# Kernel tuning notes

Hardware: AMD Instinct MI355X
Metric: run time of the kernel (lower is better)

The kernel has to match this reference:

```python
import jax, jax.numpy as jnp
import numpy as np
import math

D = 768
H = 8
DK = D // H
FF = 1024
EPS = 1e-5


def _layer_norm(x, g, b):
    m = jnp.mean(x, axis=-1, keepdims=True)
    v = jnp.mean((x - m) ** 2, axis=-1, keepdims=True)
    return (x - m) * jax.lax.rsqrt(v + EPS) * g + b


def _mha(x, attention_mask, Wq, bq, Wv, bv, g, b):
    # x: (B,S,D); attention_mask: (B,S,1) bool (True = masked/padding query row)
    B, S, _ = x.shape
    q = (x @ Wq + bq).reshape(B, S, H, DK).transpose(0, 2, 1, 3)  # (B,H,S,dk)
    # NOTE: original code uses the V projection for BOTH k and v (k = self.V(x))
    kv = (x @ Wv + bv).reshape(B, S, H, DK).transpose(0, 2, 1, 3)
    k = kv
    v = kv
    w = jnp.einsum('bhqd,bhkd->bhqk', q, k) / math.sqrt(DK)  # (B,H,S,S)
    pad = attention_mask[:, None, :, :]                      # (B,1,S,1) -> bcast (B,1,S,S)
    causal = jnp.triu(jnp.ones((S, S), dtype=bool), k=1)     # look-ahead mask
    mask = pad | causal
    w = jnp.where(mask, jnp.float32(-1e9), w)
    # NOTE: original uses nn.Softmax(dim=2) -> softmax over the QUERY axis
    score = jax.nn.softmax(w, axis=2)
    o = jnp.einsum('bhqk,bhkd->bhqd', score, v)              # (B,H,S,dk)
    o = o.transpose(0, 2, 1, 3).reshape(B, S, D)
    return _layer_norm(o + x, g, b)


def _ffn(x, W1, b1, W2, b2, g, b):
    h = jax.nn.relu(x @ W1 + b1)
    return _layer_norm(h @ W2 + b2 + x, g, b)


def setup_inputs() -> dict:
    key = jax.random.key(0)
    ks = jax.random.split(key, 16)
    B, S = 8, 1024
    sc = 0.02
    inp = {
        'x': jax.random.normal(ks[0], (B, S, D), dtype=jnp.float32),
        'attention_mask': jax.random.randint(ks[1], (B, S, 1), 0, 2).astype(bool),
    }
    for i, pre in enumerate(['a1', 'a2']):
        inp[pre + '_Wq'] = jax.random.normal(ks[2 + 4 * i], (D, D), dtype=jnp.float32) * sc
        inp[pre + '_bq'] = jnp.zeros((D,), dtype=jnp.float32)
        inp[pre + '_Wv'] = jax.random.normal(ks[3 + 4 * i], (D, D), dtype=jnp.float32) * sc
        inp[pre + '_bv'] = jnp.zeros((D,), dtype=jnp.float32)
        inp[pre + '_g'] = jnp.ones((D,), dtype=jnp.float32)
        inp[pre + '_b'] = jnp.zeros((D,), dtype=jnp.float32)
    inp['f_W1'] = jax.random.normal(ks[10], (D, FF), dtype=jnp.float32) * sc
    inp['f_b1'] = jnp.zeros((FF,), dtype=jnp.float32)
    inp['f_W2'] = jax.random.normal(ks[11], (FF, D), dtype=jnp.float32) * sc
    inp['f_b2'] = jnp.zeros((D,), dtype=jnp.float32)
    inp['f_g'] = jnp.ones((D,), dtype=jnp.float32)
    inp['f_b'] = jnp.zeros((D,), dtype=jnp.float32)
    return inp


def reference(x, attention_mask,
              a1_Wq, a1_bq, a1_Wv, a1_bv, a1_g, a1_b,
              a2_Wq, a2_bq, a2_Wv, a2_bv, a2_g, a2_b,
              f_W1, f_b1, f_W2, f_b2, f_g, f_b):
    x = _mha(x, attention_mask, a1_Wq, a1_bq, a1_Wv, a1_bv, a1_g, a1_b)
    x = _mha(x, attention_mask, a2_Wq, a2_bq, a2_Wv, a2_bv, a2_g, a2_b)
    x = _ffn(x, f_W1, f_b1, f_W2, f_b2, f_g, f_b)
    return x
```

## Files before the change

kernel.cpp:

```cpp
#include <hip/hip_runtime.h>
#include <cstddef>

#define BB 8
#define SS 1024
#define DD 768
#define HH 8
#define DKK 96
#define FFF 1024
#define MM (BB*SS)
#define QVW 1536
#define SM_SCALE 0.10206207261596577f
#define NT2 8

typedef unsigned short ushort_t;
typedef short short8 __attribute__((ext_vector_type(8)));
typedef float f32x4 __attribute__((ext_vector_type(4)));
typedef float f32x16 __attribute__((ext_vector_type(16)));
typedef ushort_t us4 __attribute__((ext_vector_type(4)));
typedef unsigned uint2v __attribute__((ext_vector_type(2)));

__device__ __forceinline__ ushort_t f2b(float f) {
    union { float f; unsigned u; } x; x.f = f;
    unsigned r = x.u + 0x7fffu + ((x.u >> 16) & 1u);
    return (ushort_t)(r >> 16);
}
__device__ __forceinline__ float b2f(ushort_t u) {
    union { unsigned u; float f; } x; x.u = ((unsigned)u) << 16;
    return x.f;
}
__device__ __forceinline__ void gload16(const ushort_t* g, void* lds_base) {
    __builtin_amdgcn_global_load_lds(
        (const __attribute__((address_space(1))) unsigned int*)g,
        (__attribute__((address_space(3))) unsigned int*)lds_base, 16, 0, 0);
}
__device__ __forceinline__ void plswap(unsigned& a, unsigned& b) {
#if __has_builtin(__builtin_amdgcn_permlane32_swap)
    uint2v r = __builtin_amdgcn_permlane32_swap(a, b, false, false);
    a = r[0]; b = r[1];
#else
    asm("v_permlane32_swap_b32 %0, %1" : "+v"(a), "+v"(b));
#endif
}

__device__ __forceinline__ void castWT_body(
    const float* __restrict__ W, ushort_t* __restrict__ Wt,
    int K, int N, int bx, int by)
{
    __shared__ float T[32][33];
    const int tx = threadIdx.x & 31, ty = threadIdx.x >> 5;
    const int n0 = bx * 32, k0 = by * 32;
    #pragma unroll
    for (int r = 0; r < 4; ++r)
        T[ty + 8*r][tx] = W[(size_t)(k0 + ty + 8*r) * N + n0 + tx];
    __syncthreads();
    #pragma unroll
    for (int r = 0; r < 4; ++r)
        Wt[(size_t)(n0 + ty + 8*r) * K + k0 + tx] = f2b(T[tx][ty + 8*r]);
}

__global__ __launch_bounds__(256) void prep_all(
    const float* __restrict__ Wqa, const float* __restrict__ Wva,
    const float* __restrict__ Wqb, const float* __restrict__ Wvb,
    ushort_t* __restrict__ Tqa, ushort_t* __restrict__ Tva,
    ushort_t* __restrict__ Tqb, ushort_t* __restrict__ Tvb,
    const float* __restrict__ W1, ushort_t* __restrict__ T1,
    const float* __restrict__ W2, ushort_t* __restrict__ T2,
    const float* __restrict__ x, ushort_t* __restrict__ xb)
{
    const int id = blockIdx.x;
    if (id < 2304) {
        const int z = id / 576, r = id % 576;
        const float* W = (z == 0) ? Wqa : (z == 1) ? Wva : (z == 2) ? Wqb : Wvb;
        ushort_t* Wt   = (z == 0) ? Tqa : (z == 1) ? Tva : (z == 2) ? Tqb : Tvb;
        castWT_body(W, Wt, DD, DD, r % 24, r / 24);
    } else if (id < 3072) {
        const int r = id - 2304;
        castWT_body(W1, T1, DD, FFF, r % 32, r / 32);
    } else if (id < 3840) {
        const int r = id - 3072;
        castWT_body(W2, T2, FFF, DD, r % 24, r / 24);
    } else {
        const int i = (id - 3840) * 256 + threadIdx.x;
        const float4 v = ((const float4*)x)[i];
        us4 o; o.x = f2b(v.x); o.y = f2b(v.y); o.z = f2b(v.z); o.w = f2b(v.w);
        ((us4*)xb)[i] = o;
    }
}

template<int RELU>
__global__ __launch_bounds__(256) void gemm_bt(
    const ushort_t* __restrict__ A, const ushort_t* __restrict__ Bt,
    const float* __restrict__ bias, const float* __restrict__ bias2, int bN,
    ushort_t* __restrict__ C, int K, int N)
{
    __shared__ ushort_t S[4*128*64];
    const int tid  = threadIdx.x;
    const int lane = tid & 63, wave = tid >> 6;
    const int wm = wave >> 1, wn = wave & 1;
    const int n = lane & 15, quad = lane >> 4;
    const int sx = n & 7;
    const int nbx = N >> 7;
    const int cpx = gridDim.x >> 3;
    const int sw  = (blockIdx.x & 7) * cpx + (blockIdx.x >> 3);
    const int bm = (sw / nbx) * 128, bn = (sw % nbx) * 128;

    f32x4 acc[4][4];
    #pragma unroll
    for (int i = 0; i < 4; ++i)
        #pragma unroll
        for (int j = 0; j < 4; ++j) acc[i][j] = (f32x4){0.f, 0.f, 0.f, 0.f};

    auto stage = [&](int k0, int buf) {
        char* abase = (char*)S + buf * 16384;
        char* bbase = (char*)S + 32768 + buf * 16384;
        #pragma unroll
        for (int it = 0; it < 4; ++it) {
            const int u   = (it*4 + wave)*64 + lane;
            const int row = u >> 3;
            const int c   = (u & 7) ^ (row & 7);
            gload16(A  + (size_t)(bm + row) * K + k0 + c*8, abase + (it*4 + wave)*1024);
            gload16(Bt + (size_t)(bn + row) * K + k0 + c*8, bbase + (it*4 + wave)*1024);
        }
    };

    stage(0, 0);
    __syncthreads();
    int cur = 0;
    for (int k0 = 0; k0 < K; k0 += 64) {
        if (k0 + 64 < K) stage(k0 + 64, cur ^ 1);
        const ushort_t* As = S + cur * 8192;
        const ushort_t* Bs = S + 16384 + cur * 8192;
        #pragma unroll
        for (int ks = 0; ks < 2; ++ks) {
            short8 af[4], bf[4];
            #pragma unroll
            for (int i = 0; i < 4; ++i)
                af[i] = *(short8*)&As[((wm*64 + i*16 + n)*8 + ((ks*4 + quad) ^ sx))*8];
            #pragma unroll
            for (int j = 0; j < 4; ++j)
                bf[j] = *(short8*)&Bs[((wn*64 + j*16 + n)*8 + ((ks*4 + quad) ^ sx))*8];
            __builtin_amdgcn_s_setprio(1);
            #pragma unroll
            for (int i = 0; i < 4; ++i)
                #pragma unroll
                for (int j = 0; j < 4; ++j)
                    acc[i][j] = __builtin_amdgcn_mfma_f32_16x16x32_bf16(af[i], bf[j], acc[i][j], 0, 0, 0);
            __builtin_amdgcn_s_setprio(0);
        }
        __syncthreads();
        cur ^= 1;
    }
    #pragma unroll
    for (int j = 0; j < 4; ++j) {
        const int col = wn*64 + j*16 + n;
        const int gcol = bn + col;
        const float bsv = (gcol < bN) ? bias[gcol] : bias2[gcol - bN];
        #pragma unroll
        for (int i = 0; i < 4; ++i) {
            const int lrow = wm*64 + i*16 + quad*4;
            #pragma unroll
            for (int r = 0; r < 4; ++r) {
                float v = acc[i][j][r] + bsv;
                if (RELU) v = fmaxf(v, 0.f);
                S[(lrow + r)*136 + col] = f2b(v);
            }
        }
    }
    __syncthreads();
    #pragma unroll
    for (int it = 0; it < 8; ++it) {
        const int u = it*256 + tid;
        const int grow = u >> 4, gc = u & 15;
        *(short8*)(C + (size_t)(bm + grow)*N + bn + gc*8) = *(short8*)&S[grow*136 + gc*8];
    }
}

__global__ __launch_bounds__(512) void attn_sums(
    const ushort_t* __restrict__ QV, const int* __restrict__ amask,
    float* __restrict__ lpart)
{
    __shared__ ushort_t Qs[128*128];
    __shared__ ushort_t Ks[2][64*128];
    __shared__ float colsum[2][8][64];
    const int tid = threadIdx.x, lane = tid & 63, wave = tid >> 6;
    const int n = lane & 15, quad = lane >> 4, sx = n & 7;
    const int hwid = blockIdx.x;
    const int v = (hwid & 7) * 32 + (hwid >> 3);
    const int px = v & 3, h = (v >> 2) & 7, b = v >> 5;
    const ushort_t* Qh = QV + (size_t)b*SS*QVW + h*DKK;
    const ushort_t* Kh = QV + (size_t)b*SS*QVW + DD + h*DKK;
    float* lpq = lpart + (size_t)(b*HH + h)*NT2*SS;

    #pragma unroll
    for (int half = 0; half < 2; ++half) {
        const int qt2 = half ? (7 - px) : px;
        const int q0 = qt2 * 128;
        const int ktmax = 2*qt2 + 1;
        #pragma unroll
        for (int it = 0; it < 4; ++it) {
            const int u = (it*8 + wave)*64 + lane;
            const int row = u >> 4, c = (u & 15) ^ (row & 7);
            if (c < 12)
                gload16(Qh + (size_t)(q0 + row)*QVW + c*8, (char*)Qs + (it*8 + wave)*1024);
        }
        const int4 mv = *(const int4*)&amask[b*SS + q0 + wave*16 + quad*4];
        const int mr[4] = {mv.x, mv.y, mv.z, mv.w};
        #pragma unroll
        for (int it = 0; it < 2; ++it) {
            const int u = (it*8 + wave)*64 + lane;
            const int row = u >> 4, c = (u & 15) ^ (row & 7);
            if (c < 12)
                gload16(Kh + (size_t)row*QVW + c*8, (char*)Ks[0] + (it*8 + wave)*1024);
        }
        __syncthreads();
        short8 aq[3];
        #pragma unroll
        for (int ks = 0; ks < 3; ++ks)
            aq[ks] = *(short8*)&Qs[((wave*16 + n)*16 + ((ks*4 + quad) ^ sx))*8];

        int cur = 0;
        for (int kt = 0; kt <= ktmax; ++kt) {
            const int k0 = kt * 64;
            if (kt < ktmax) {
                #pragma unroll
                for (int it = 0; it < 2; ++it) {
                    const int u = (it*8 + wave)*64 + lane;
                    const int row = u >> 4, c = (u & 15) ^ (row & 7);
                    if (c < 12)
                        gload16(Kh + (size_t)(k0 + 64 + row)*QVW + c*8,
                                (char*)Ks[cur^1] + (it*8 + wave)*1024);
                }
            }
            if (kt > 0 && tid < 64) {
                const float s = colsum[cur^1][0][tid] + colsum[cur^1][1][tid]
                              + colsum[cur^1][2][tid] + colsum[cur^1][3][tid]
                              + colsum[cur^1][4][tid] + colsum[cur^1][5][tid]
                              + colsum[cur^1][6][tid] + colsum[cur^1][7][tid];
                lpq[(size_t)qt2*SS + (k0 - 64) + tid] = s;
            }
            #pragma unroll
            for (int ns = 0; ns < 4; ++ns) {
                f32x4 sa = (f32x4){0.f, 0.f, 0.f, 0.f};
                __builtin_amdgcn_s_setprio(1);
                #pragma unroll
                for (int ks = 0; ks < 3; ++ks) {
                    const short8 bk = *(short8*)&Ks[cur][((ns*16 + n)*16 + ((ks*4 + quad) ^ sx))*8];
                    sa = __builtin_amdgcn_mfma_f32_16x16x32_bf16(aq[ks], bk, sa, 0, 0, 0);
                }
                __builtin_amdgcn_s_setprio(0);
                const int kl = ns*16 + n;
                const int keyg = k0 + kl;
                float s = 0.f;
                #pragma unroll
                for (int r = 0; r < 4; ++r) {
                    const int qg = q0 + wave*16 + quad*4 + r;
                    const bool dead = (mr[r] != 0) || (keyg > qg);
                    s += dead ? 0.f : __expf(sa[r] * SM_SCALE);
                }
                s += __shfl_xor(s, 16);
                s += __shfl_xor(s, 32);
                if (quad == 0) colsum[cur][wave][kl] = s;
            }
            __syncthreads();
            cur ^= 1;
        }
        if (tid < 64) {
            const int pb = ktmax & 1;
            const float s = colsum[pb][0][tid] + colsum[pb][1][tid]
                          + colsum[pb][2][tid] + colsum[pb][3][tid]
                          + colsum[pb][4][tid] + colsum[pb][5][tid]
                          + colsum[pb][6][tid] + colsum[pb][7][tid];
            lpq[(size_t)qt2*SS + ktmax*64 + tid] = s;
        }
    }
}

__global__ __launch_bounds__(256) void transpose_scale(
    const ushort_t* __restrict__ QV, const float* __restrict__ lpart,
    ushort_t* __restrict__ Vt)
{
    __shared__ ushort_t T[64][104];
    __shared__ float rlv[64];
    const int tid = threadIdx.x;
    const int k0 = blockIdx.x * 64, h = blockIdx.y, b = blockIdx.z;
    const ushort_t* src = QV + (size_t)b*SS*QVW + DD + h*DKK;
    for (int s = tid; s < 768; s += 256) {
        const int r = s / 12, c = s % 12;
        *(short8*)&T[r][c*8] = *(const short8*)(src + (size_t)(k0 + r)*QVW + c*8);
    }
    if (tid < 64) {
        const float* lp = lpart + (size_t)(b*HH + h)*NT2*SS;
        float l = 0.f;
        for (int qt2 = k0 >> 7; qt2 < NT2; ++qt2) l += lp[(size_t)qt2*SS + k0 + tid];
        rlv[tid] = (l > 0.f) ? (1.f / l) : 0.f;
    }
    __syncthreads();
    ushort_t* dst = Vt + ((size_t)b*HH + h)*DKK*SS;
    for (int s = tid; s < 768; s += 256) {
        const int dk = s >> 3, c = s & 7;
        short8 v;
        #pragma unroll
        for (int i = 0; i < 8; ++i)
            v[i] = (short)f2b(b2f(T[c*8 + i][dk]) * rlv[c*8 + i]);
        *(short8*)(dst + (size_t)dk*SS + k0 + c*8) = v;
    }
}

__global__ __launch_bounds__(256, 2) void attn_pv_re(
    const ushort_t* __restrict__ QV, const int* __restrict__ amask,
    const ushort_t* __restrict__ Vt, ushort_t* __restrict__ O)
{
    __shared__ ushort_t Ks[2][64*128];
    __shared__ ushort_t Vs[2][96*64];
    const int tid = threadIdx.x, lane = tid & 63, wave = tid >> 6;
    const int ln31 = lane & 31, hi = lane >> 5;
    const int hwid = blockIdx.x;
    const int v = (hwid & 7) * 32 + (hwid >> 3);
    const int px = v & 3, h = (v >> 2) & 7, b = v >> 5;
    const ushort_t* Qh = QV + (size_t)b*SS*QVW + h*DKK;
    const ushort_t* Kh = QV + (size_t)b*SS*QVW + DD + h*DKK;
    const ushort_t* Vth = Vt + ((size_t)b*HH + h)*DKK*SS;

    #pragma unroll
    for (int half = 0; half < 2; ++half) {
        const int qt2 = half ? (7 - px) : px;
        const int q0 = qt2 * 128;
        const int ktmax = 2*qt2 + 1;
        const int qrow = q0 + wave*32 + ln31;
        short8 bq[6];
        #pragma unroll
        for (int t = 0; t < 6; ++t)
            bq[t] = *(const short8*)(Qh + (size_t)qrow*QVW + t*16 + hi*8);
        const bool padq = amask[b*SS + qrow] != 0;

        #pragma unroll
        for (int it = 0; it < 4; ++it) {
            const int u = (it*4 + wave)*64 + lane;
            const int row = u >> 4, c = (u & 15) ^ (row & 7);
            if (c < 12)
                gload16(Kh + (size_t)row*QVW + c*8, (char*)Ks[0] + (it*4 + wave)*1024);
        }
        #pragma unroll
        for (int it = 0; it < 3; ++it) {
            const int u = (it*4 + wave)*64 + lane;
            const int row = u >> 3, c = (u & 7) ^ (row & 7);
            gload16(Vth + (size_t)row*SS + c*8, (char*)Vs[0] + (it*4 + wave)*1024);
        }
        __syncthreads();

        f32x16 acc[3];
        #pragma unroll
        for (int db = 0; db < 3; ++db)
            #pragma unroll
            for (int i = 0; i < 16; ++i) acc[db][i] = 0.f;

        int cur = 0;
        for (int kt = 0; kt <= ktmax; ++kt) {
            const int k0 = kt * 64;
            if (kt < ktmax) {
                #pragma unroll
                for (int it = 0; it < 4; ++it) {
                    const int u = (it*4 + wave)*64 + lane;
                    const int row = u >> 4, c = (u & 15) ^ (row & 7);
                    if (c < 12)
                        gload16(Kh + (size_t)(k0 + 64 + row)*QVW + c*8,
                                (char*)Ks[cur^1] + (it*4 + wave)*1024);
                }
                #pragma unroll
                for (int it = 0; it < 3; ++it) {
                    const int u = (it*4 + wave)*64 + lane;
                    const int row = u >> 3, c = (u & 7) ^ (row & 7);
                    gload16(Vth + (size_t)row*SS + k0 + 64 + c*8,
                            (char*)Vs[cur^1] + (it*4 + wave)*1024);
                }
            }
            #pragma unroll
            for (int kb = 0; kb < 2; ++kb) {
                f32x16 sk;
                #pragma unroll
                for (int i = 0; i < 16; ++i) sk[i] = 0.f;
                const int krow = kb*32 + ln31;
                __builtin_amdgcn_s_setprio(1);
                #pragma unroll
                for (int t = 0; t < 6; ++t) {
                    const short8 ak = *(short8*)&Ks[cur][krow*128 + (((t*2 + hi) ^ (krow & 7))*8)];
                    sk = __builtin_amdgcn_mfma_f32_32x32x16_bf16(ak, bq[t], sk, 0, 0, 0);
                }
                __builtin_amdgcn_s_setprio(0);
                const int kbase = k0 + kb*32 + 4*hi;
                float p[16];
                #pragma unroll
                for (int r = 0; r < 16; ++r) {
                    const int kg = kbase + (r & 3) + 8*(r >> 2);
                    const bool dead = padq || (kg > qrow);
                    p[r] = dead ? 0.f : __expf(sk[r] * SM_SCALE);
                }
                unsigned w[8];
                #pragma unroll
                for (int i = 0; i < 8; ++i)
                    asm("v_cvt_pk_bf16_f32 %0, %1, %2" : "=v"(w[i]) : "v"(p[2*i]), "v"(p[2*i+1]));
                plswap(w[0], w[2]);
                plswap(w[1], w[3]);
                plswap(w[4], w[6]);
                plswap(w[5], w[7]);
                __builtin_amdgcn_s_setprio(1);
                #pragma unroll
                for (int s = 0; s < 2; ++s) {
                    short8 ae;
                    unsigned* aeu = (unsigned*)&ae;
                    aeu[0] = w[s*4 + 0]; aeu[1] = w[s*4 + 1];
                    aeu[2] = w[s*4 + 2]; aeu[3] = w[s*4 + 3];
                    #pragma unroll
                    for (int db = 0; db < 3; ++db) {
                        const int drow = db*32 + ln31;
                        const short8 bv = *(short8*)&Vs[cur][drow*64 + (((kb*4 + s*2 + hi) ^ (drow & 7))*8)];
                        acc[db] = __builtin_amdgcn_mfma_f32_32x32x16_bf16(ae, bv, acc[db], 0, 0, 0);
                    }
                }
                __builtin_amdgcn_s_setprio(0);
            }
            __syncthreads();
            cur ^= 1;
        }
        #pragma unroll
        for (int db = 0; db < 3; ++db) {
            #pragma unroll
            for (int r = 0; r < 16; ++r) {
                const int q = q0 + wave*32 + (r & 3) + 8*(r >> 2) + 4*hi;
                O[((size_t)b*SS + q)*DD + h*DKK + db*32 + ln31] = f2b(acc[db][r]);
            }
        }
    }
}

__device__ __forceinline__ float block_sum256(float s, float* tmp4)
{
    #pragma unroll
    for (int off = 32; off > 0; off >>= 1) s += __shfl_down(s, off);
    __syncthreads();
    if ((threadIdx.x & 63) == 0) tmp4[threadIdx.x >> 6] = s;
    __syncthreads();
    return tmp4[0] + tmp4[1] + tmp4[2] + tmp4[3];
}

template<int XBF, int RBF, int OUTF32>
__global__ __launch_bounds__(256) void resid_ln(
    const void* __restrict__ X, const void* __restrict__ R,
    const float* __restrict__ g, const float* __restrict__ beta,
    ushort_t* __restrict__ OutB, float* __restrict__ OutF)
{
    __shared__ float tmp4[4];
    const int row = blockIdx.x;
    const int tid = threadIdx.x;
    float v[3], s = 0.f;
    #pragma unroll
    for (int i = 0; i < 3; ++i) {
        const size_t idx = (size_t)row * DD + tid + 256*i;
        const float xv = XBF ? b2f(((const ushort_t*)X)[idx]) : ((const float*)X)[idx];
        const float rv = RBF ? b2f(((const ushort_t*)R)[idx]) : ((const float*)R)[idx];
        v[i] = xv + rv;
        s += v[i];
    }
    const float mu = block_sum256(s, tmp4) * (1.f / DD);
    float qv = 0.f;
    #pragma unroll
    for (int i = 0; i < 3; ++i) { const float d = v[i] - mu; qv += d * d; }
    const float inv = rsqrtf(block_sum256(qv, tmp4) * (1.f / DD) + 1e-5f);
    #pragma unroll
    for (int i = 0; i < 3; ++i) {
        const int c = tid + 256*i;
        const float o = (v[i] - mu) * inv * g[c] + beta[c];
        if (OUTF32) OutF[(size_t)row * DD + c] = o;
        else        OutB[(size_t)row * DD + c] = f2b(o);
    }
}

extern "C" void kernel_launch(void* const* d_in, const int* in_sizes, int n_in,
                              void* d_out, int out_size, void* d_ws, size_t ws_size,
                              hipStream_t stream)
{
    (void)in_sizes; (void)n_in; (void)out_size; (void)ws_size;
    const float* x0    = (const float*)d_in[0];
    const int*   amask = (const int*)d_in[1];
    const float* a1_Wq = (const float*)d_in[2];
    const float* a1_bq = (const float*)d_in[3];
    const float* a1_Wv = (const float*)d_in[4];
    const float* a1_bv = (const float*)d_in[5];
    const float* a1_g  = (const float*)d_in[6];
    const float* a1_b  = (const float*)d_in[7];
    const float* a2_Wq = (const float*)d_in[8];
    const float* a2_bq = (const float*)d_in[9];
    const float* a2_Wv = (const float*)d_in[10];
    const float* a2_bv = (const float*)d_in[11];
    const float* a2_g  = (const float*)d_in[12];
    const float* a2_b  = (const float*)d_in[13];
    const float* f_W1  = (const float*)d_in[14];
    const float* f_b1  = (const float*)d_in[15];
    const float* f_W2  = (const float*)d_in[16];
    const float* f_b2  = (const float*)d_in[17];
    const float* f_g   = (const float*)d_in[18];
    const float* f_b   = (const float*)d_in[19];

    char* ws = (char*)d_ws;
    size_t off = 0;
    auto alloc = [&](size_t bytes) { void* p = ws + off; off += (bytes + 255) & ~(size_t)255; return p; };
    ushort_t* WqvT1 = (ushort_t*)alloc((size_t)QVW*DD*2);
    ushort_t* WqvT2 = (ushort_t*)alloc((size_t)QVW*DD*2);
    ushort_t* W1T   = (ushort_t*)alloc((size_t)DD*FFF*2);
    ushort_t* W2T   = (ushort_t*)alloc((size_t)DD*FFF*2);
    ushort_t* xb0   = (ushort_t*)alloc((size_t)MM*DD*2);
    ushort_t* xb1   = (ushort_t*)alloc((size_t)MM*DD*2);
    ushort_t* xb2   = (ushort_t*)alloc((size_t)MM*DD*2);
    ushort_t* Ob    = (ushort_t*)alloc((size_t)MM*DD*2);
    ushort_t* QVb   = (ushort_t*)alloc((size_t)MM*QVW*2);
    ushort_t* hb    = QVb;
    ushort_t* Vtb   = (ushort_t*)alloc((size_t)MM*DD*2);
    float* lpart = (float*)alloc((size_t)BB*HH*NT2*SS*4);
    float* out = (float*)d_out;

    const dim3 blk(256);
    const dim3 blk512(512);
    const dim3 gat(256);
    const dim3 gtr(SS/64, HH, BB);

    prep_all<<<dim3(9984), blk, 0, stream>>>(
        a1_Wq, a1_Wv, a2_Wq, a2_Wv,
        WqvT1, WqvT1 + (size_t)DD*DD, WqvT2, WqvT2 + (size_t)DD*DD,
        f_W1, W1T, f_W2, W2T, x0, xb0);

    gemm_bt<0><<<dim3((QVW/128)*(MM/128)), blk, 0, stream>>>(xb0, WqvT1, a1_bq, a1_bv, DD, QVb, DD, QVW);
    attn_sums<<<gat, blk512, 0, stream>>>(QVb, amask, lpart);
    transpose_scale<<<gtr, blk, 0, stream>>>(QVb, lpart, Vtb);
    attn_pv_re<<<gat, blk, 0, stream>>>(QVb, amask, Vtb, Ob);
    resid_ln<1,0,0><<<dim3(MM), blk, 0, stream>>>(Ob, x0, a1_g, a1_b, xb1, nullptr);

    gemm_bt<0><<<dim3((QVW/128)*(MM/128)), blk, 0, stream>>>(xb1, WqvT2, a2_bq, a2_bv, DD, QVb, DD, QVW);
    attn_sums<<<gat, blk512, 0, stream>>>(QVb, amask, lpart);
    transpose_scale<<<gtr, blk, 0, stream>>>(QVb, lpart, Vtb);
    attn_pv_re<<<gat, blk, 0, stream>>>(QVb, amask, Vtb, Ob);
    resid_ln<1,1,0><<<dim3(MM), blk, 0, stream>>>(Ob, xb1, a2_g, a2_b, xb2, nullptr);

    gemm_bt<1><<<dim3((FFF/128)*(MM/128)), blk, 0, stream>>>(xb2, W1T, f_b1, f_b1, FFF, hb, DD, FFF);
    gemm_bt<0><<<dim3((DD/128)*(MM/128)), blk, 0, stream>>>(hb, W2T, f_b2, f_b2, DD, Ob, FFF, DD);
    resid_ln<1,1,1><<<dim3(MM), blk, 0, stream>>>(Ob, xb2, f_g, f_b, nullptr, out);
}
```

Baseline: 377.9 us.

## Run both causal query tiles concurrently in 512-thread attention PV blocks

The PV attention kernel used to process its two paired query tiles (short and long causal spans) one after the other in a 256-thread block. Now it uses a 512-thread block where two 4-wave groups each take one tile at the same time, with separate double-buffered K/V shared-memory tiles per group. The loop runs to the longer tile's extent and the short group idles while still joining the barriers. This raises per-block parallelism and removes the serial second pass. In exchange it doubles LDS per block, drops to one block per CU in the launch bounds, and leaves the short-tile waves idle during the tail.

Result: no change. 372.4 us (-1.5%).

```diff
diff --git a/kernel.cpp b/kernel.cpp
--- a/kernel.cpp
+++ b/kernel.cpp
@@ -306,13 +306,14 @@
     }
 }
 
-__global__ __launch_bounds__(256, 2) void attn_pv_re(
+__global__ __launch_bounds__(512, 1) void attn_pv_re(
     const ushort_t* __restrict__ QV, const int* __restrict__ amask,
     const ushort_t* __restrict__ Vt, ushort_t* __restrict__ O)
 {
-    __shared__ ushort_t Ks[2][64*128];
-    __shared__ ushort_t Vs[2][96*64];
+    __shared__ ushort_t Ks[2][2][64*128];
+    __shared__ ushort_t Vs[2][2][96*64];
     const int tid = threadIdx.x, lane = tid & 63, wave = tid >> 6;
+    const int grp = wave >> 2, w4 = wave & 3;
     const int ln31 = lane & 31, hi = lane >> 5;
     const int hwid = blockIdx.x;
     const int v = (hwid & 7) * 32 + (hwid >> 3);
@@ -321,59 +322,59 @@
     const ushort_t* Kh = QV + (size_t)b*SS*QVW + DD + h*DKK;
     const ushort_t* Vth = Vt + ((size_t)b*HH + h)*DKK*SS;
 
-    #pragma unroll
-    for (int half = 0; half < 2; ++half) {
-        const int qt2 = half ? (7 - px) : px;
-        const int q0 = qt2 * 128;
-        const int ktmax = 2*qt2 + 1;
-        const int qrow = q0 + wave*32 + ln31;
-        short8 bq[6];
-        #pragma unroll
-        for (int t = 0; t < 6; ++t)
-            bq[t] = *(const short8*)(Qh + (size_t)qrow*QVW + t*16 + hi*8);
-        const bool padq = amask[b*SS + qrow] != 0;
-
-        #pragma unroll
-        for (int it = 0; it < 4; ++it) {
-            const int u = (it*4 + wave)*64 + lane;
-            const int row = u >> 4, c = (u & 15) ^ (row & 7);
-            if (c < 12)
-                gload16(Kh + (size_t)row*QVW + c*8, (char*)Ks[0] + (it*4 + wave)*1024);
-        }
-        #pragma unroll
-        for (int it = 0; it < 3; ++it) {
-            const int u = (it*4 + wave)*64 + lane;
-            const int row = u >> 3, c = (u & 7) ^ (row & 7);
-            gload16(Vth + (size_t)row*SS + c*8, (char*)Vs[0] + (it*4 + wave)*1024);
-        }
-        __syncthreads();
-
-        f32x16 acc[3];
-        #pragma unroll
-        for (int db = 0; db < 3; ++db)
-            #pragma unroll
-            for (int i = 0; i < 16; ++i) acc[db][i] = 0.f;
-
-        int cur = 0;
-        for (int kt = 0; kt <= ktmax; ++kt) {
-            const int k0 = kt * 64;
-            if (kt < ktmax) {
-                #pragma unroll
-                for (int it = 0; it < 4; ++it) {
-                    const int u = (it*4 + wave)*64 + lane;
-                    const int row = u >> 4, c = (u & 15) ^ (row & 7);
-                    if (c < 12)
-                        gload16(Kh + (size_t)(k0 + 64 + row)*QVW + c*8,
-                                (char*)Ks[cur^1] + (it*4 + wave)*1024);
-                }
-                #pragma unroll
-                for (int it = 0; it < 3; ++it) {
-                    const int u = (it*4 + wave)*64 + lane;
-                    const int row = u >> 3, c = (u & 7) ^ (row & 7);
-                    gload16(Vth + (size_t)row*SS + k0 + 64 + c*8,
-                            (char*)Vs[cur^1] + (it*4 + wave)*1024);
-                }
-            }
+    const int qt2 = grp ? (7 - px) : px;
+    const int q0 = qt2 * 128;
+    const int ktmax = 2*qt2 + 1;
+    const int ktend = 2*(7 - px) + 1;
+    const int qrow = q0 + w4*32 + ln31;
+    short8 bq[6];
+    #pragma unroll
+    for (int t = 0; t < 6; ++t)
+        bq[t] = *(const short8*)(Qh + (size_t)qrow*QVW + t*16 + hi*8);
+    const bool padq = amask[b*SS + qrow] != 0;
+
+    #pragma unroll
+    for (int it = 0; it < 4; ++it) {
+        const int u = (it*4 + w4)*64 + lane;
+        const int row = u >> 4, c = (u & 15) ^ (row & 7);
+        if (c < 12)
+            gload16(Kh + (size_t)row*QVW + c*8, (char*)Ks[grp][0] + (it*4 + w4)*1024);
+    }
+    #pragma unroll
+    for (int it = 0; it < 3; ++it) {
+        const int u = (it*4 + w4)*64 + lane;
+        const int row = u >> 3, c = (u & 7) ^ (row & 7);
+        gload16(Vth + (size_t)row*SS + c*8, (char*)Vs[grp][0] + (it*4 + w4)*1024);
+    }
+    __syncthreads();
+
+    f32x16 acc[3];
+    #pragma unroll
+    for (int db = 0; db < 3; ++db)
+        #pragma unroll
+        for (int i = 0; i < 16; ++i) acc[db][i] = 0.f;
+
+    int cur = 0;
+    for (int kt = 0; kt <= ktend; ++kt) {
+        const int k0 = kt * 64;
+        if (kt < ktmax) {
+            #pragma unroll
+            for (int it = 0; it < 4; ++it) {
+                const int u = (it*4 + w4)*64 + lane;
+                const int row = u >> 4, c = (u & 15) ^ (row & 7);
+                if (c < 12)
+                    gload16(Kh + (size_t)(k0 + 64 + row)*QVW + c*8,
+                            (char*)Ks[grp][cur^1] + (it*4 + w4)*1024);
+            }
+            #pragma unroll
+            for (int it = 0; it < 3; ++it) {
+                const int u = (it*4 + w4)*64 + lane;
+                const int row = u >> 3, c = (u & 7) ^ (row & 7);
+                gload16(Vth + (size_t)row*SS + k0 + 64 + c*8,
+                        (char*)Vs[grp][cur^1] + (it*4 + w4)*1024);
+            }
+        }
+        if (kt <= ktmax) {
             #pragma unroll
             for (int kb = 0; kb < 2; ++kb) {
                 f32x16 sk;
@@ -383,7 +384,7 @@
                 __builtin_amdgcn_s_setprio(1);
                 #pragma unroll
                 for (int t = 0; t < 6; ++t) {
-                    const short8 ak = *(short8*)&Ks[cur][krow*128 + (((t*2 + hi) ^ (krow & 7))*8)];
+                    const short8 ak = *(short8*)&Ks[grp][cur][krow*128 + (((t*2 + hi) ^ (krow & 7))*8)];
                     sk = __builtin_amdgcn_mfma_f32_32x32x16_bf16(ak, bq[t], sk, 0, 0, 0);
                 }
                 __builtin_amdgcn_s_setprio(0);
@@ -413,22 +414,22 @@
                     #pragma unroll
                     for (int db = 0; db < 3; ++db) {
                         const int drow = db*32 + ln31;
-                        const short8 bv = *(short8*)&Vs[cur][drow*64 + (((kb*4 + s*2 + hi) ^ (drow & 7))*8)];
+                        const short8 bv = *(short8*)&Vs[grp][cur][drow*64 + (((kb*4 + s*2 + hi) ^ (drow & 7))*8)];
                         acc[db] = __builtin_amdgcn_mfma_f32_32x32x16_bf16(ae, bv, acc[db], 0, 0, 0);
                     }
                 }
                 __builtin_amdgcn_s_setprio(0);
             }
-            __syncthreads();
-            cur ^= 1;
-        }
-        #pragma unroll
-        for (int db = 0; db < 3; ++db) {
-            #pragma unroll
-            for (int r = 0; r < 16; ++r) {
-                const int q = q0 + wave*32 + (r & 3) + 8*(r >> 2) + 4*hi;
-                O[((size_t)b*SS + q)*DD + h*DKK + db*32 + ln31] = f2b(acc[db][r]);
-            }
+        }
+        __syncthreads();
+        cur ^= 1;
+    }
+    #pragma unroll
+    for (int db = 0; db < 3; ++db) {
+        #pragma unroll
+        for (int r = 0; r < 16; ++r) {
+            const int q = q0 + w4*32 + (r & 3) + 8*(r >> 2) + 4*hi;
+            O[((size_t)b*SS + q)*DD + h*DKK + db*32 + ln31] = f2b(acc[db][r]);
         }
     }
 }
@@ -531,13 +532,13 @@
     gemm_bt<0><<<dim3((QVW/128)*(MM/128)), blk, 0, stream>>>(xb0, WqvT1, a1_bq, a1_bv, DD, QVb, DD, QVW);
     attn_sums<<<gat, blk512, 0, stream>>>(QVb, amask, lpart);
     transpose_scale<<<gtr, blk, 0, stream>>>(QVb, lpart, Vtb);
-    attn_pv_re<<<gat, blk, 0, stream>>>(QVb, amask, Vtb, Ob);
+    attn_pv_re<<<gat, blk512, 0, stream>>>(QVb, amask, Vtb, Ob);
     resid_ln<1,0,0><<<dim3(MM), blk, 0, stream>>>(Ob, x0, a1_g, a1_b, xb1, nullptr);
 
     gemm_bt<0><<<dim3((QVW/128)*(MM/128)), blk, 0, stream>>>(xb1, WqvT2, a2_bq, a2_bv, DD, QVb, DD, QVW);
     attn_sums<<<gat, blk512, 0, stream>>>(QVb, amask, lpart);
     transpose_scale<<<gtr, blk, 0, stream>>>(QVb, lpart, Vtb);
-    attn_pv_re<<<gat, blk, 0, stream>>>(QVb, amask, Vtb, Ob);
+    attn_pv_re<<<gat, blk512, 0, stream>>>(QVb, amask, Vtb, Ob);
     resid_ln<1,1,0><<<dim3(MM), blk, 0, stream>>>(Ob, xb1, a2_g, a2_b, xb2, nullptr);
 
     gemm_bt<1><<<dim3((FFF/128)*(MM/128)), blk, 0, stream>>>(xb2, W1T, f_b1, f_b1, FFF, hb, DD, FFF);
```
